# Kernel optimization log

Hardware: AMD Instinct MI355X
Metric: run time of the kernel (lower is better)

Reference implementation:

```python
import jax, jax.numpy as jnp
import numpy as np

B, N, DIM = 4, 2048, 1024
HEADS, DIM_HEAD = 16, 64
INNER = HEADS * DIM_HEAD  # 1024
SCALE = DIM_HEAD ** -0.5


def setup_inputs() -> dict:
    key = jax.random.key(0)
    k_x, k_qkv, k_out, k_b = jax.random.split(key, 4)
    x = jax.random.normal(k_x, (B, N, DIM), dtype=jnp.float32)
    # nn.Linear weights, stored transposed for x @ W convenience
    w_qkv = jax.random.normal(k_qkv, (DIM, 3 * INNER), dtype=jnp.float32) * (DIM ** -0.5)
    w_out = jax.random.normal(k_out, (INNER, DIM), dtype=jnp.float32) * (INNER ** -0.5)
    b_out = jax.random.normal(k_b, (DIM,), dtype=jnp.float32) * 0.01
    return {"x": x, "w_qkv": w_qkv, "w_out": w_out, "b_out": b_out}


def _split_heads(t):
    # 'b n (h d) -> (b h) n d'
    b, n, _ = t.shape
    return t.reshape(b, n, HEADS, DIM_HEAD).transpose(0, 2, 1, 3).reshape(b * HEADS, n, DIM_HEAD)


def reference(x, w_qkv, w_out, b_out):
    b, n, _ = x.shape
    qkv = x @ w_qkv  # [b, n, 3*inner]
    q, k, v = jnp.split(qkv, 3, axis=-1)
    q = q * SCALE
    q, k, v = map(_split_heads, (q, k, v))  # [(b h), n, d]
    sim = jnp.einsum('bid,bjd->bij', q, k)  # [(b h), n, n]
    a = jax.nn.softmax(sim, axis=-1)
    out = jnp.einsum('bij,bjd->bid', a, v)  # [(b h), n, d]
    # '(b h) n d -> b n (h d)'
    out = out.reshape(b, HEADS, n, DIM_HEAD).transpose(0, 2, 1, 3).reshape(b, n, INNER)
    return out @ w_out + b_out  # dropout p=0.0 is identity
```

## Files before the change

kernel.cpp:

```cpp
#include <hip/hip_runtime.h>
#include <stdint.h>


typedef uint16_t u16;
typedef __bf16 bf16x8 __attribute__((ext_vector_type(8)));
typedef float f32x4 __attribute__((ext_vector_type(4)));
typedef unsigned u32x2 __attribute__((ext_vector_type(2)));
typedef unsigned u32x4 __attribute__((ext_vector_type(4)));

#define AS3(p) ((__attribute__((address_space(3))) uint32_t*)(p))
#define AS1(p) ((const __attribute__((address_space(1))) uint32_t*)(p))

__device__ __forceinline__ void gl_lds16(const void* g, void* lds) {
  __builtin_amdgcn_global_load_lds(AS1(g), AS3(lds), 16, 0, 0);
}

__device__ __forceinline__ u16 f2bf(float f) {
  union { __bf16 b; u16 u; } x; x.b = (__bf16)f;
  return x.u;
}

__global__ void cvt_f32_bf16(const float* __restrict__ in, u16* __restrict__ out, long n) {
  long i = ((long)blockIdx.x * 256 + threadIdx.x) * 8;
  if (i >= n) return;
  u16 r[8];
  #pragma unroll
  for (int j = 0; j < 8; ++j) r[j] = f2bf(in[i + j]);
  *(uint4*)(out + i) = *(const uint4*)r;
}

__global__ void transpose2_f2b(const float* __restrict__ in0, u16* __restrict__ out0,
                               const float* __restrict__ in1, u16* __restrict__ out1,
                               int C0, int C1) {
  const int R = 1024;
  const float* in = blockIdx.z ? in1 : in0;
  u16* out = blockIdx.z ? out1 : out0;
  int C = blockIdx.z ? C1 : C0;
  int c0 = blockIdx.x * 32;
  if (c0 >= C) return;
  __shared__ u16 tile[32][33];
  int tx = threadIdx.x, ty = threadIdx.y;
  int r0 = blockIdx.y * 32;
  #pragma unroll
  for (int i = 0; i < 4; ++i)
    tile[ty + 8 * i][tx] = f2bf(in[(long)(r0 + ty + 8 * i) * C + c0 + tx]);
  __syncthreads();
  #pragma unroll
  for (int i = 0; i < 4; ++i)
    out[(long)(c0 + ty + 8 * i) * R + r0 + tx] = tile[tx][ty + 8 * i];
}

template <bool BIAS, bool OUTF32>
__global__ __launch_bounds__(256) void gemm_bt(const u16* __restrict__ A, const u16* __restrict__ Bt,
                                               const float* __restrict__ bias, void* __restrict__ Cv,
                                               int M, int N, int K, int qcols, float qscale) {
  __shared__ u16 sA[128 * 64];
  __shared__ u16 sB[128 * 64];
  const int tid = threadIdx.x;
  const int w = tid >> 6, l = tid & 63;
  const int l15 = l & 15, lh = l >> 4;
  const int wr = w >> 1, wc = w & 1;
  int bid = blockIdx.x + blockIdx.y * gridDim.x;
  int xcd = bid & 7, idx = bid >> 3;
  int by = xcd * (gridDim.y >> 3) + idx / gridDim.x;
  int bx = idx % gridDim.x;
  const long row0 = (long)by * 128, col0 = (long)bx * 128;

  const f32x4 fzero = {0.f, 0.f, 0.f, 0.f};
  f32x4 acc[4][4];
  #pragma unroll
  for (int m = 0; m < 4; ++m)
    #pragma unroll
    for (int n = 0; n < 4; ++n) acc[m][n] = fzero;

  for (int kt = 0; kt < K; kt += 64) {
    __syncthreads();
    #pragma unroll
    for (int i = 0; i < 4; ++i) {
      int c = w * 256 + i * 64 + l;
      int row = c >> 3, sub = c & 7;
      int col8 = (sub ^ (row & 7)) * 8;
      gl_lds16(A + (row0 + row) * K + kt + col8, (void*)(sA + w * 2048 + i * 512));
      gl_lds16(Bt + (col0 + row) * K + kt + col8, (void*)(sB + w * 2048 + i * 512));
    }
    __syncthreads();
    #pragma unroll
    for (int ks = 0; ks < 2; ++ks) {
      bf16x8 a[4], b[4];
      #pragma unroll
      for (int m = 0; m < 4; ++m) {
        int row = wr * 64 + m * 16 + l15;
        a[m] = *(const bf16x8*)&sA[row * 64 + ((ks * 32 + lh * 8) ^ ((row & 7) << 3))];
      }
      #pragma unroll
      for (int n = 0; n < 4; ++n) {
        int row = wc * 64 + n * 16 + l15;
        b[n] = *(const bf16x8*)&sB[row * 64 + ((ks * 32 + lh * 8) ^ ((row & 7) << 3))];
      }
      __builtin_amdgcn_s_setprio(1);
      #pragma unroll
      for (int m = 0; m < 4; ++m)
        #pragma unroll
        for (int n = 0; n < 4; ++n)
          acc[m][n] = __builtin_amdgcn_mfma_f32_16x16x32_bf16(a[m], b[n], acc[m][n], 0, 0, 0);
      __builtin_amdgcn_s_setprio(0);
    }
  }

  #pragma unroll
  for (int n = 0; n < 4; ++n) {
    long col = col0 + wc * 64 + n * 16 + l15;
    float bv = 0.f;
    if (BIAS) bv = bias[col];
    float scl = (col < qcols) ? qscale : 1.0f;
    #pragma unroll
    for (int m = 0; m < 4; ++m) {
      #pragma unroll
      for (int r = 0; r < 4; ++r) {
        long row = row0 + wr * 64 + m * 16 + lh * 4 + r;
        if (OUTF32) ((float*)Cv)[row * N + col] = acc[m][n][r] + bv;
        else        ((u16*)Cv)[row * N + col] = f2bf(acc[m][n][r] * scl + bv);
      }
    }
  }
}

__global__ __launch_bounds__(512, 4) void attn_k(const u16* __restrict__ qkv, u16* __restrict__ attn) {
  __shared__ u16 smem[24576];
  const int tid = threadIdx.x;
  const int w = tid >> 6, l = tid & 63;
  const int l15 = l & 15, lh = l >> 4;
  const int b = blockIdx.x >> 4, h = blockIdx.x & 15;
  const int qt = blockIdx.y;
  const long rs = 3072;
  const long qrow0 = (long)b * 2048 + qt * 256;
  const u16* Qg    = qkv + qrow0 * rs + h * 64;
  const u16* Kbase = qkv + (long)b * 2048 * rs + 1024 + h * 64;
  const u16* Vbase = qkv + (long)b * 2048 * rs + 2048 + h * 64;

  #pragma unroll
  for (int i = 0; i < 4; ++i) {
    int c = (w * 4 + i) * 64 + l;
    int row = c >> 3;
    int col8 = ((c & 7) ^ (row & 7)) * 8;
    gl_lds16(Qg + (long)row * rs + col8, (void*)(smem + (w * 4 + i) * 512));
  }
  {
    int row = tid >> 3, sub = tid & 7;
    int col8 = (sub ^ (row & 7)) * 8;
    gl_lds16(Kbase + (long)row * rs + col8, (void*)(smem + 16384 + w * 512));

    int kv0 = (tid & 31) * 2, d0 = (tid >> 5) * 4;
    const u16* Vg = Vbase + (long)kv0 * rs + d0;
    u32x2 va = *(const u32x2*)Vg;
    u32x2 vb = *(const u32x2*)(Vg + rs);
    const u16* pa = (const u16*)&va;
    const u16* pb = (const u16*)&vb;
    #pragma unroll
    for (int jj = 0; jj < 4; ++jj) {
      int d = d0 + jj;
      *(uint32_t*)&smem[20480 + d * 64 + (kv0 ^ ((d & 7) << 3))] =
          (uint32_t)pa[jj] | ((uint32_t)pb[jj] << 16);
    }
  }
  __syncthreads();

  bf16x8 aq[2][2];
  #pragma unroll
  for (int m = 0; m < 2; ++m)
    #pragma unroll
    for (int ks = 0; ks < 2; ++ks) {
      int row = w * 32 + m * 16 + l15;
      aq[m][ks] = *(const bf16x8*)&smem[row * 64 + ((ks * 32 + lh * 8) ^ ((row & 7) << 3))];
    }
  __syncthreads();

  bf16x8 ones;
  { union { u32x4 u; bf16x8 f; } cv; cv.u = (u32x4){0x3F803F80u, 0x3F803F80u, 0x3F803F80u, 0x3F803F80u}; ones = cv.f; }

  const f32x4 fzero = {0.f, 0.f, 0.f, 0.f};
  f32x4 acc[2][4];
  f32x4 acc_l[2];
  #pragma unroll
  for (int m = 0; m < 2; ++m) {
    acc_l[m] = fzero;
    #pragma unroll
    for (int n = 0; n < 4; ++n) acc[m][n] = fzero;
  }

  for (int t = 0; t < 32; ++t) {
    const int kOff  = (t & 1) ? 0     : 16384;
    const int vOff  = (t & 1) ? 4096  : 20480;
    const int kOffN = (t & 1) ? 16384 : 0;
    const int vOffN = (t & 1) ? 20480 : 4096;

    u32x2 va, vb;
    int kv0 = (tid & 31) * 2, d0v = (tid >> 5) * 4;
    if (t < 31) {
      int row = tid >> 3, sub = tid & 7;
      int col8 = (sub ^ (row & 7)) * 8;
      gl_lds16(Kbase + ((long)(t + 1) * 64 + row) * rs + col8, (void*)(smem + kOffN + w * 512));
      const u16* Vg = Vbase + ((long)(t + 1) * 64 + kv0) * rs + d0v;
      va = *(const u32x2*)Vg;
      vb = *(const u32x2*)(Vg + rs);
    }

    f32x4 s[2][4];
    #pragma unroll
    for (int m = 0; m < 2; ++m)
      #pragma unroll
      for (int n = 0; n < 4; ++n) s[m][n] = fzero;
    #pragma unroll
    for (int ks = 0; ks < 2; ++ks) {
      bf16x8 bk[4];
      #pragma unroll
      for (int n = 0; n < 4; ++n) {
        int row = n * 16 + l15;
        bk[n] = *(const bf16x8*)&smem[kOff + row * 64 + ((ks * 32 + lh * 8) ^ ((row & 7) << 3))];
      }
      __builtin_amdgcn_s_setprio(1);
      #pragma unroll
      for (int m = 0; m < 2; ++m)
        #pragma unroll
        for (int n = 0; n < 4; ++n)
          s[m][n] = __builtin_amdgcn_mfma_f32_16x16x32_bf16(bk[n], aq[m][ks], s[m][n], 0, 0, 0);
      __builtin_amdgcn_s_setprio(0);
    }

    unsigned Wm[2][4][2];
    #pragma unroll
    for (int m = 0; m < 2; ++m) {
      #pragma unroll
      for (int n = 0; n < 4; ++n) {
        float p0 = __builtin_amdgcn_exp2f(s[m][n][0]);
        float p1 = __builtin_amdgcn_exp2f(s[m][n][1]);
        float p2 = __builtin_amdgcn_exp2f(s[m][n][2]);
        float p3 = __builtin_amdgcn_exp2f(s[m][n][3]);
        Wm[m][n][0] = (unsigned)f2bf(p0) | ((unsigned)f2bf(p1) << 16);
        Wm[m][n][1] = (unsigned)f2bf(p2) | ((unsigned)f2bf(p3) << 16);
      }
    }

    #pragma unroll
    for (int ks = 0; ks < 2; ++ks) {
      bf16x8 pf[2];
      #pragma unroll
      for (int m = 0; m < 2; ++m) {
        unsigned a0 = Wm[m][2 * ks][0], b0 = Wm[m][2 * ks + 1][0];
        unsigned a1 = Wm[m][2 * ks][1], b1 = Wm[m][2 * ks + 1][1];
        asm("v_permlane32_swap_b32 %0, %1" : "+v"(a0), "+v"(b0));
        asm("v_permlane16_swap_b32 %0, %1" : "+v"(a0), "+v"(b0));
        asm("v_permlane32_swap_b32 %0, %1" : "+v"(a1), "+v"(b1));
        asm("v_permlane16_swap_b32 %0, %1" : "+v"(a1), "+v"(b1));
        union { u32x4 u; bf16x8 f; } cv;
        cv.u = (u32x4){a0, a1, b0, b1};
        pf[m] = cv.f;
      }
      bf16x8 bv4[4];
      #pragma unroll
      for (int n = 0; n < 4; ++n) {
        int vr = n * 16 + l15;
        bv4[n] = *(const bf16x8*)&smem[vOff + vr * 64 + ((ks * 32 + lh * 8) ^ ((vr & 7) << 3))];
      }
      __builtin_amdgcn_s_setprio(1);
      #pragma unroll
      for (int n = 0; n < 4; ++n)
        #pragma unroll
        for (int m = 0; m < 2; ++m)
          acc[m][n] = __builtin_amdgcn_mfma_f32_16x16x32_bf16(bv4[n], pf[m], acc[m][n], 0, 0, 0);
      #pragma unroll
      for (int m = 0; m < 2; ++m)
        acc_l[m] = __builtin_amdgcn_mfma_f32_16x16x32_bf16(ones, pf[m], acc_l[m], 0, 0, 0);
      __builtin_amdgcn_s_setprio(0);
    }

    if (t < 31) {
      const u16* pa = (const u16*)&va;
      const u16* pb = (const u16*)&vb;
      #pragma unroll
      for (int jj = 0; jj < 4; ++jj) {
        int d = d0v + jj;
        *(uint32_t*)&smem[vOffN + d * 64 + (kv0 ^ ((d & 7) << 3))] =
            (uint32_t)pa[jj] | ((uint32_t)pb[jj] << 16);
      }
      __syncthreads();
    }
  }

  #pragma unroll
  for (int m = 0; m < 2; ++m) {
    float inv = 1.0f / acc_l[m][0];
    long q = qrow0 + w * 32 + m * 16 + l15;
    #pragma unroll
    for (int n = 0; n < 4; ++n) {
      unsigned lo = (unsigned)f2bf(acc[m][n][0] * inv) | ((unsigned)f2bf(acc[m][n][1] * inv) << 16);
      unsigned hi = (unsigned)f2bf(acc[m][n][2] * inv) | ((unsigned)f2bf(acc[m][n][3] * inv) << 16);
      *(u32x2*)&attn[q * 1024 + h * 64 + n * 16 + lh * 4] = (u32x2){lo, hi};
    }
  }
}

extern "C" void kernel_launch(void* const* d_in, const int* in_sizes, int n_in,
                              void* d_out, int out_size, void* d_ws, size_t ws_size,
                              hipStream_t stream) {
  (void)in_sizes; (void)n_in; (void)out_size; (void)ws_size;
  const float* x     = (const float*)d_in[0];
  const float* w_qkv = (const float*)d_in[1];
  const float* w_out = (const float*)d_in[2];
  const float* b_out = (const float*)d_in[3];
  float* out = (float*)d_out;

  u16* ws    = (u16*)d_ws;
  u16* wqkvT = ws;
  u16* woutT = wqkvT + (size_t)3072 * 1024;
  u16* xbf   = woutT + (size_t)1024 * 1024;
  u16* qkv   = xbf   + (size_t)8192 * 1024;
  u16* attnb = qkv   + (size_t)8192 * 3072;

  const float QSCALE = 0.125f * 1.44269504088896f;

  cvt_f32_bf16<<<4096, 256, 0, stream>>>(x, xbf, (long)8192 * 1024);
  transpose2_f2b<<<dim3(96, 32, 2), dim3(32, 8), 0, stream>>>(w_qkv, wqkvT, w_out, woutT, 3072, 1024);
  gemm_bt<false, false><<<dim3(24, 64), 256, 0, stream>>>(xbf, wqkvT, nullptr, qkv,
                                                          8192, 3072, 1024, 1024, QSCALE);
  attn_k<<<dim3(64, 8), 512, 0, stream>>>(qkv, attnb);
  gemm_bt<true, true><<<dim3(8, 64), 256, 0, stream>>>(attnb, woutT, b_out, out,
                                                       8192, 1024, 1024, 0, 1.0f);
}
```

Before: 190.4 us.

## Unroll attention loop by two, hoist LDS offsets, stage K through registers

The KV loop is unrolled by two so the double-buffer offsets become compile-time constants, and the swizzled LDS read/write offsets and global base pointers are computed once before the loop. The next-tile K load no longer uses a global-to-LDS direct load. It now goes through registers, is issued after the QK MFMAs, and is written to LDS at the end of the iteration, matching how V is staged. The aim is to cut per-iteration address arithmetic and overlap global loads with the softmax and PV math, at the cost of more VGPRs that could hurt occupancy.

```diff
diff --git a/kernel.cpp b/kernel.cpp
--- a/kernel.cpp
+++ b/kernel.cpp
@@ -138,6 +138,26 @@
   const u16* Kbase = qkv + (long)b * 2048 * rs + 1024 + h * 64;
   const u16* Vbase = qkv + (long)b * 2048 * rs + 2048 + h * 64;
 
+  const int krow = tid >> 3, ksub = tid & 7;
+  const int kWrOff = krow * 64 + (ksub ^ (krow & 7)) * 8;
+  const int kv0 = (tid & 31) * 2, d0v = (tid >> 5) * 4;
+  int vWrOff[4];
+  #pragma unroll
+  for (int jj = 0; jj < 4; ++jj) {
+    int d = d0v + jj;
+    vWrOff[jj] = d * 64 + (kv0 ^ ((d & 7) << 3));
+  }
+  int rdOff[2][4];
+  #pragma unroll
+  for (int ks = 0; ks < 2; ++ks)
+    #pragma unroll
+    for (int n = 0; n < 4; ++n) {
+      int row = n * 16 + l15;
+      rdOff[ks][n] = row * 64 + ((ks * 32 + lh * 8) ^ ((row & 7) << 3));
+    }
+  const u16* Kg0 = Kbase + (long)krow * rs + ksub * 8;
+  const u16* Vg0 = Vbase + (long)kv0 * rs + d0v;
+
   #pragma unroll
   for (int i = 0; i < 4; ++i) {
     int c = (w * 4 + i) * 64 + l;
@@ -146,22 +166,15 @@
     gl_lds16(Qg + (long)row * rs + col8, (void*)(smem + (w * 4 + i) * 512));
   }
   {
-    int row = tid >> 3, sub = tid & 7;
-    int col8 = (sub ^ (row & 7)) * 8;
-    gl_lds16(Kbase + (long)row * rs + col8, (void*)(smem + 16384 + w * 512));
-
-    int kv0 = (tid & 31) * 2, d0 = (tid >> 5) * 4;
-    const u16* Vg = Vbase + (long)kv0 * rs + d0;
-    u32x2 va = *(const u32x2*)Vg;
-    u32x2 vb = *(const u32x2*)(Vg + rs);
+    int col8 = (ksub ^ (krow & 7)) * 8;
+    gl_lds16(Kbase + (long)krow * rs + col8, (void*)(smem + 16384 + w * 512));
+    u32x2 va = *(const u32x2*)Vg0;
+    u32x2 vb = *(const u32x2*)(Vg0 + rs);
     const u16* pa = (const u16*)&va;
     const u16* pb = (const u16*)&vb;
     #pragma unroll
-    for (int jj = 0; jj < 4; ++jj) {
-      int d = d0 + jj;
-      *(uint32_t*)&smem[20480 + d * 64 + (kv0 ^ ((d & 7) << 3))] =
-          (uint32_t)pa[jj] | ((uint32_t)pb[jj] << 16);
-    }
+    for (int jj = 0; jj < 4; ++jj)
+      *(uint32_t*)&smem[20480 + vWrOff[jj]] = (uint32_t)pa[jj] | ((uint32_t)pb[jj] << 16);
   }
   __syncthreads();
 
@@ -188,104 +201,94 @@
     for (int n = 0; n < 4; ++n) acc[m][n] = fzero;
   }
 
-  for (int t = 0; t < 32; ++t) {
-    const int kOff  = (t & 1) ? 0     : 16384;
-    const int vOff  = (t & 1) ? 4096  : 20480;
-    const int kOffN = (t & 1) ? 16384 : 0;
-    const int vOffN = (t & 1) ? 20480 : 4096;
-
-    u32x2 va, vb;
-    int kv0 = (tid & 31) * 2, d0v = (tid >> 5) * 4;
-    if (t < 31) {
-      int row = tid >> 3, sub = tid & 7;
-      int col8 = (sub ^ (row & 7)) * 8;
-      gl_lds16(Kbase + ((long)(t + 1) * 64 + row) * rs + col8, (void*)(smem + kOffN + w * 512));
-      const u16* Vg = Vbase + ((long)(t + 1) * 64 + kv0) * rs + d0v;
-      va = *(const u32x2*)Vg;
-      vb = *(const u32x2*)(Vg + rs);
-    }
-
-    f32x4 s[2][4];
-    #pragma unroll
-    for (int m = 0; m < 2; ++m)
-      #pragma unroll
-      for (int n = 0; n < 4; ++n) s[m][n] = fzero;
-    #pragma unroll
-    for (int ks = 0; ks < 2; ++ks) {
-      bf16x8 bk[4];
-      #pragma unroll
-      for (int n = 0; n < 4; ++n) {
-        int row = n * 16 + l15;
-        bk[n] = *(const bf16x8*)&smem[kOff + row * 64 + ((ks * 32 + lh * 8) ^ ((row & 7) << 3))];
-      }
-      __builtin_amdgcn_s_setprio(1);
-      #pragma unroll
-      for (int m = 0; m < 2; ++m)
-        #pragma unroll
-        for (int n = 0; n < 4; ++n)
-          s[m][n] = __builtin_amdgcn_mfma_f32_16x16x32_bf16(bk[n], aq[m][ks], s[m][n], 0, 0, 0);
-      __builtin_amdgcn_s_setprio(0);
-    }
-
-    unsigned Wm[2][4][2];
-    #pragma unroll
-    for (int m = 0; m < 2; ++m) {
-      #pragma unroll
-      for (int n = 0; n < 4; ++n) {
-        float p0 = __builtin_amdgcn_exp2f(s[m][n][0]);
-        float p1 = __builtin_amdgcn_exp2f(s[m][n][1]);
-        float p2 = __builtin_amdgcn_exp2f(s[m][n][2]);
-        float p3 = __builtin_amdgcn_exp2f(s[m][n][3]);
-        Wm[m][n][0] = (unsigned)f2bf(p0) | ((unsigned)f2bf(p1) << 16);
-        Wm[m][n][1] = (unsigned)f2bf(p2) | ((unsigned)f2bf(p3) << 16);
-      }
-    }
-
-    #pragma unroll
-    for (int ks = 0; ks < 2; ++ks) {
-      bf16x8 pf[2];
-      #pragma unroll
-      for (int m = 0; m < 2; ++m) {
-        unsigned a0 = Wm[m][2 * ks][0], b0 = Wm[m][2 * ks + 1][0];
-        unsigned a1 = Wm[m][2 * ks][1], b1 = Wm[m][2 * ks + 1][1];
-        asm("v_permlane32_swap_b32 %0, %1" : "+v"(a0), "+v"(b0));
-        asm("v_permlane16_swap_b32 %0, %1" : "+v"(a0), "+v"(b0));
-        asm("v_permlane32_swap_b32 %0, %1" : "+v"(a1), "+v"(b1));
-        asm("v_permlane16_swap_b32 %0, %1" : "+v"(a1), "+v"(b1));
-        union { u32x4 u; bf16x8 f; } cv;
-        cv.u = (u32x4){a0, a1, b0, b1};
-        pf[m] = cv.f;
-      }
-      bf16x8 bv4[4];
-      #pragma unroll
-      for (int n = 0; n < 4; ++n) {
-        int vr = n * 16 + l15;
-        bv4[n] = *(const bf16x8*)&smem[vOff + vr * 64 + ((ks * 32 + lh * 8) ^ ((vr & 7) << 3))];
-      }
-      __builtin_amdgcn_s_setprio(1);
-      #pragma unroll
-      for (int n = 0; n < 4; ++n)
-        #pragma unroll
-        for (int m = 0; m < 2; ++m)
-          acc[m][n] = __builtin_amdgcn_mfma_f32_16x16x32_bf16(bv4[n], pf[m], acc[m][n], 0, 0, 0);
-      #pragma unroll
-      for (int m = 0; m < 2; ++m)
-        acc_l[m] = __builtin_amdgcn_mfma_f32_16x16x32_bf16(ones, pf[m], acc_l[m], 0, 0, 0);
-      __builtin_amdgcn_s_setprio(0);
-    }
-
-    if (t < 31) {
-      const u16* pa = (const u16*)&va;
-      const u16* pb = (const u16*)&vb;
-      #pragma unroll
-      for (int jj = 0; jj < 4; ++jj) {
-        int d = d0v + jj;
-        *(uint32_t*)&smem[vOffN + d * 64 + (kv0 ^ ((d & 7) << 3))] =
-            (uint32_t)pa[jj] | ((uint32_t)pb[jj] << 16);
-      }
-      __syncthreads();
-    }
-  }
+#define ATTN_TILE(T, KO, VO, KON, VON)                                                   \
+  {                                                                                      \
+    f32x4 s[2][4];                                                                       \
+    _Pragma("unroll")                                                                    \
+    for (int m = 0; m < 2; ++m)                                                          \
+      _Pragma("unroll")                                                                  \
+      for (int n = 0; n < 4; ++n) s[m][n] = fzero;                                       \
+    _Pragma("unroll")                                                                    \
+    for (int ks = 0; ks < 2; ++ks) {                                                     \
+      bf16x8 bk[4];                                                                      \
+      _Pragma("unroll")                                                                  \
+      for (int n = 0; n < 4; ++n)                                                        \
+        bk[n] = *(const bf16x8*)&smem[(KO) + rdOff[ks][n]];                              \
+      __builtin_amdgcn_s_setprio(1);                                                     \
+      _Pragma("unroll")                                                                  \
+      for (int m = 0; m < 2; ++m)                                                        \
+        _Pragma("unroll")                                                                \
+        for (int n = 0; n < 4; ++n)                                                      \
+          s[m][n] = __builtin_amdgcn_mfma_f32_16x16x32_bf16(bk[n], aq[m][ks], s[m][n], 0, 0, 0); \
+      __builtin_amdgcn_s_setprio(0);                                                     \
+    }                                                                                    \
+    uint4 kreg;                                                                          \
+    u32x2 va, vb;                                                                        \
+    if ((T) < 31) {                                                                      \
+      kreg = *(const uint4*)(Kg0 + (long)((T) + 1) * 64 * rs);                           \
+      const u16* Vg = Vg0 + (long)((T) + 1) * 64 * rs;                                   \
+      va = *(const u32x2*)Vg;                                                            \
+      vb = *(const u32x2*)(Vg + rs);                                                     \
+    }                                                                                    \
+    unsigned Wm[2][4][2];                                                                \
+    _Pragma("unroll")                                                                    \
+    for (int m = 0; m < 2; ++m) {                                                        \
+      _Pragma("unroll")                                                                  \
+      for (int n = 0; n < 4; ++n) {                                                      \
+        float p0 = __builtin_amdgcn_exp2f(s[m][n][0]);                                   \
+        float p1 = __builtin_amdgcn_exp2f(s[m][n][1]);                                   \
+        float p2 = __builtin_amdgcn_exp2f(s[m][n][2]);                                   \
+        float p3 = __builtin_amdgcn_exp2f(s[m][n][3]);                                   \
+        Wm[m][n][0] = (unsigned)f2bf(p0) | ((unsigned)f2bf(p1) << 16);                   \
+        Wm[m][n][1] = (unsigned)f2bf(p2) | ((unsigned)f2bf(p3) << 16);                   \
+      }                                                                                  \
+    }                                                                                    \
+    _Pragma("unroll")                                                                    \
+    for (int ks = 0; ks < 2; ++ks) {                                                     \
+      bf16x8 pf[2];                                                                      \
+      _Pragma("unroll")                                                                  \
+      for (int m = 0; m < 2; ++m) {                                                      \
+        unsigned a0 = Wm[m][2 * ks][0], b0 = Wm[m][2 * ks + 1][0];                       \
+        unsigned a1 = Wm[m][2 * ks][1], b1 = Wm[m][2 * ks + 1][1];                       \
+        asm("v_permlane32_swap_b32 %0, %1" : "+v"(a0), "+v"(b0));                        \
+        asm("v_permlane16_swap_b32 %0, %1" : "+v"(a0), "+v"(b0));                        \
+        asm("v_permlane32_swap_b32 %0, %1" : "+v"(a1), "+v"(b1));                        \
+        asm("v_permlane16_swap_b32 %0, %1" : "+v"(a1), "+v"(b1));                        \
+        union { u32x4 u; bf16x8 f; } cv;                                                 \
+        cv.u = (u32x4){a0, a1, b0, b1};                                                  \
+        pf[m] = cv.f;                                                                    \
+      }                                                                                  \
+      bf16x8 bv4[4];                                                                     \
+      _Pragma("unroll")                                                                  \
+      for (int n = 0; n < 4; ++n)                                                        \
+        bv4[n] = *(const bf16x8*)&smem[(VO) + rdOff[ks][n]];                             \
+      __builtin_amdgcn_s_setprio(1);                                                     \
+      _Pragma("unroll")                                                                  \
+      for (int n = 0; n < 4; ++n)                                                        \
+        _Pragma("unroll")                                                                \
+        for (int m = 0; m < 2; ++m)                                                      \
+          acc[m][n] = __builtin_amdgcn_mfma_f32_16x16x32_bf16(bv4[n], pf[m], acc[m][n], 0, 0, 0); \
+      _Pragma("unroll")                                                                  \
+      for (int m = 0; m < 2; ++m)                                                        \
+        acc_l[m] = __builtin_amdgcn_mfma_f32_16x16x32_bf16(ones, pf[m], acc_l[m], 0, 0, 0); \
+      __builtin_amdgcn_s_setprio(0);                                                     \
+    }                                                                                    \
+    if ((T) < 31) {                                                                      \
+      *(uint4*)&smem[(KON) + kWrOff] = kreg;                                             \
+      const u16* pa = (const u16*)&va;                                                   \
+      const u16* pb = (const u16*)&vb;                                                   \
+      _Pragma("unroll")                                                                  \
+      for (int jj = 0; jj < 4; ++jj)                                                     \
+        *(uint32_t*)&smem[(VON) + vWrOff[jj]] = (uint32_t)pa[jj] | ((uint32_t)pb[jj] << 16); \
+      __syncthreads();                                                                   \
+    }                                                                                    \
+  }
+
+  for (int t = 0; t < 32; t += 2) {
+    ATTN_TILE(t,     16384, 20480, 0,     4096)
+    ATTN_TILE(t + 1, 0,     4096,  16384, 20480)
+  }
+#undef ATTN_TILE
 
   #pragma unroll
   for (int m = 0; m < 2; ++m) {
```

Measured after the change: 203.4 us. +6.9%, slower.
